# Performance work log

Measured on AMD Instinct MI355X. Metric: run time of the kernel, lower is better.

The kernel has to match this reference:

```python
import jax, jax.numpy as jnp
import numpy as np

K = 3        # neighborhood kernel per spatial dim
DIL = 1      # dilation per spatial dim
NH = 8       # num heads
C = 64       # embed dims
EPS = 1e-5   # InstanceNorm eps


def _interp_axis(x, axis, out_len):
    # 1D linear interpolation with align_corners=True semantics
    in_len = x.shape[axis]
    pos = jnp.arange(out_len, dtype=jnp.float32) * ((in_len - 1) / (out_len - 1))
    i0 = jnp.clip(jnp.floor(pos).astype(jnp.int32), 0, in_len - 2)
    w = pos - i0.astype(jnp.float32)
    shape = [1] * x.ndim
    shape[axis] = out_len
    w = w.reshape(shape)
    return jnp.take(x, i0, axis=axis) * (1.0 - w) + jnp.take(x, i0 + 1, axis=axis) * w


def _upsample2_trilinear(x):
    # separable trilinear upsample x2 over the three spatial axes (2,3,4)
    for ax in (2, 3, 4):
        x = _interp_axis(x, ax, 2 * x.shape[ax])
    return x


def _instance_norm(t):
    # InstanceNorm3d, affine=False: normalize per (B,C) over spatial dims
    m = jnp.mean(t, axis=(2, 3, 4), keepdims=True)
    v = jnp.var(t, axis=(2, 3, 4), keepdims=True)
    return (t - m) * jax.lax.rsqrt(v + EPS)


def _nbr_idx(L, k, d):
    # NATTEN-style clamped neighborhood: window shifts to stay in-bounds at edges
    i = np.arange(L)
    start = np.clip(i - d * (k // 2), 0, L - d * (k - 1) - 1)
    idx = start[:, None] + np.arange(k)[None, :] * d          # (L,k) absolute nbr index
    rel = (idx - i[:, None]) // d + (k - 1)                   # (L,k) rel-pos-bias index in [0,2k-2]
    return jnp.asarray(idx), jnp.asarray(rel)


def _nca3d(qs, kv, Wq, bq, Wk, bk, Wv, bv, Wo, bo, rpb):
    # qs, kv: (B,H,W,Z,C) channels-last; q from skip, k/v from upsampled x
    B, H, W, Z, Cc = qs.shape
    dh = Cc // NH
    scale = dh ** -0.5
    q = (qs @ Wq + bq).reshape(B, H, W, Z, NH, dh) * scale
    k = (kv @ Wk + bk).reshape(B, H, W, Z, NH, dh)
    v = (kv @ Wv + bv).reshape(B, H, W, Z, NH, dh)

    ih, rh = _nbr_idx(H, K, DIL)
    iw, rw = _nbr_idx(W, K, DIL)
    iz, rz = _nbr_idx(Z, K, DIL)

    def gather_nbrs(t):
        t = jnp.take(t, ih, axis=1)   # (B,H,k,W,Z,nh,dh)
        t = jnp.take(t, iw, axis=3)   # (B,H,k,W,k,Z,nh,dh)
        t = jnp.take(t, iz, axis=5)   # (B,H,k,W,k,Z,k,nh,dh)
        t = jnp.transpose(t, (0, 1, 3, 5, 7, 2, 4, 6, 8))
        return t.reshape(B, H, W, Z, NH, K * K * K, dh)

    kg = gather_nbrs(k)
    vg = gather_nbrs(v)

    logits = jnp.einsum('bxyzhd,bxyzhmd->bxyzhm', q, kg)  # (B,H,W,Z,nh,27)

    # relative position bias: rpb (nh, 2k-1, 2k-1, 2k-1) gathered per query position
    bias = rpb[:, rh]                    # (nh,H,k,2k-1,2k-1)
    bias = jnp.take(bias, rw, axis=3)    # (nh,H,k,W,k,2k-1)
    bias = jnp.take(bias, rz, axis=5)    # (nh,H,k,W,k,Z,k)
    bias = jnp.transpose(bias, (1, 3, 5, 0, 2, 4, 6)).reshape(H, W, Z, NH, K * K * K)

    attn = jax.nn.softmax(logits + bias, axis=-1)
    o = jnp.einsum('bxyzhm,bxyzhmd->bxyzhd', attn, vg).reshape(B, H, W, Z, Cc)
    o = o @ Wo + bo
    return jnp.transpose(o, (0, 4, 1, 2, 3))  # back to (B,C,H,W,Z)


def setup_inputs() -> dict:
    key = jax.random.key(0)
    ks = jax.random.split(key, 8)
    s = 1.0 / np.sqrt(C)
    inp = {
        'x': jax.random.normal(ks[0], (1, C, 32, 32, 8), dtype=jnp.float32),
        'skip': jax.random.normal(ks[1], (1, C, 64, 64, 16), dtype=jnp.float32),
        'Wq': jax.random.normal(ks[2], (C, C), dtype=jnp.float32) * s,
        'bq': jnp.zeros((C,), dtype=jnp.float32),
        'Wk': jax.random.normal(ks[3], (C, C), dtype=jnp.float32) * s,
        'bk': jnp.zeros((C,), dtype=jnp.float32),
        'Wv': jax.random.normal(ks[4], (C, C), dtype=jnp.float32) * s,
        'bv': jnp.zeros((C,), dtype=jnp.float32),
        'Wo': jax.random.normal(ks[5], (C, C), dtype=jnp.float32) * s,
        'bo': jnp.zeros((C,), dtype=jnp.float32),
        'rpb': jax.random.normal(ks[6], (NH, 2 * K - 1, 2 * K - 1, 2 * K - 1), dtype=jnp.float32) * 0.02,
    }
    return inp


def reference(x, skip, Wq, bq, Wk, bk, Wv, bv, Wo, bo, rpb):
    xu = _instance_norm(_upsample2_trilinear(x))   # (B,C,2H,2W,2Z) == skip shape
    sk = _instance_norm(skip)
    qs = jnp.transpose(sk, (0, 2, 3, 4, 1))        # queries from skip
    kv = jnp.transpose(xu, (0, 2, 3, 4, 1))        # keys/values from upsampled x
    return _nca3d(qs, kv, Wq, bq, Wk, bk, Wv, bv, Wo, bo, rpb)
```

## Files before the change

kernel.cpp:

```cpp
#include <hip/hip_runtime.h>
#include <hip/hip_bf16.h>

typedef __hip_bfloat16 bf16;
typedef __attribute__((ext_vector_type(8))) short short8;

static constexpr int NPOS = 65536;

__device__ __forceinline__ float bs2f(short s) {
  union { float f; unsigned u; } cv;
  cv.u = ((unsigned)(unsigned short)s) << 16;
  return cv.f;
}
__device__ __forceinline__ short f2bs(float f) {
  bf16 b = __float2bfloat16(f);
  short r;
  __builtin_memcpy(&r, &b, 2);
  return r;
}

__global__ __launch_bounds__(256) void k_partial(const float* __restrict__ x,
                                                 const float* __restrict__ skip,
                                                 bf16* __restrict__ xu,
                                                 float* __restrict__ partials) {
  __shared__ float s1[256];
  __shared__ float s2[256];
  int b = blockIdx.x, tid = threadIdx.x;
  float sum = 0.f, sq = 0.f;
  if (b < 1024) {
    int c = b >> 4;
    int h = (b & 15) * 4 + (tid >> 6);
    int w = tid & 63;
    float fh = (float)h * (31.0f / 63.0f);
    int ih = (int)fh; if (ih > 30) ih = 30;
    float wh = fh - (float)ih;
    float fw = (float)w * (31.0f / 63.0f);
    int iw = (int)fw; if (iw > 30) iw = 30;
    float ww = fw - (float)iw;
    const float* base = x + c * 8192 + ih * 256 + iw * 8;
    float4 A0 = *(const float4*)(base);
    float4 A1 = *(const float4*)(base + 4);
    float4 B0 = *(const float4*)(base + 8);
    float4 B1 = *(const float4*)(base + 12);
    float4 C0 = *(const float4*)(base + 256);
    float4 C1 = *(const float4*)(base + 260);
    float4 D0 = *(const float4*)(base + 264);
    float4 D1 = *(const float4*)(base + 268);
    float ra[8] = {A0.x, A0.y, A0.z, A0.w, A1.x, A1.y, A1.z, A1.w};
    float rb[8] = {B0.x, B0.y, B0.z, B0.w, B1.x, B1.y, B1.z, B1.w};
    float rc[8] = {C0.x, C0.y, C0.z, C0.w, C1.x, C1.y, C1.z, C1.w};
    float rd[8] = {D0.x, D0.y, D0.z, D0.w, D1.x, D1.y, D1.z, D1.w};
    short8 o0, o1;
#pragma unroll
    for (int z = 0; z < 16; z++) {
      float fz = (float)z * (7.0f / 15.0f);
      int iz = (int)fz; if (iz > 6) iz = 6;
      float wz = fz - (float)iz;
      float va = ra[iz] * (1.f - wz) + ra[iz + 1] * wz;
      float vb = rb[iz] * (1.f - wz) + rb[iz + 1] * wz;
      float vc = rc[iz] * (1.f - wz) + rc[iz + 1] * wz;
      float vd = rd[iz] * (1.f - wz) + rd[iz + 1] * wz;
      float v0 = va * (1.f - ww) + vb * ww;
      float v1 = vc * (1.f - ww) + vd * ww;
      float v = v0 * (1.f - wh) + v1 * wh;
      sum += v; sq += v * v;
      if (z < 8) o0[z] = f2bs(v); else o1[z - 8] = f2bs(v);
    }
    bf16* xo = xu + (size_t)c * NPOS + h * 1024 + w * 16;
    *(short8*)xo = o0;
    *(short8*)(xo + 8) = o1;
  } else {
    int bb = b - 1024;
    const float4* p =
        (const float4*)(skip + (size_t)(bb >> 4) * NPOS + (bb & 15) * 4096);
    for (int i = tid; i < 1024; i += 256) {
      float4 v = p[i];
      sum += v.x + v.y + v.z + v.w;
      sq += v.x * v.x + v.y * v.y + v.z * v.z + v.w * v.w;
    }
  }
  s1[tid] = sum; s2[tid] = sq;
  __syncthreads();
  for (int s = 128; s > 0; s >>= 1) {
    if (tid < s) { s1[tid] += s1[tid + s]; s2[tid] += s2[tid + s]; }
    __syncthreads();
  }
  if (tid == 0) { partials[2 * b] = s1[0]; partials[2 * b + 1] = s2[0]; }
}

__global__ __launch_bounds__(128) void k_finalize(const float* __restrict__ partials,
                                                  float* __restrict__ stats) {
  int t = threadIdx.x;
  int base = (t < 64) ? t * 16 : 1024 + (t - 64) * 16;
  float sum = 0.f, sq = 0.f;
#pragma unroll
  for (int j = 0; j < 16; j++) {
    sum += partials[2 * (base + j)];
    sq  += partials[2 * (base + j) + 1];
  }
  float m = sum * (1.0f / NPOS);
  float var = sq * (1.0f / NPOS) - m * m;
  int off = (t < 64) ? 0 : 128;
  int c = t & 63;
  stats[off + c] = m;
  stats[off + 64 + c] = rsqrtf(var + 1e-5f);
}

__global__ __launch_bounds__(256) void k_proj_kvq(
    const bf16* __restrict__ xu, const float* __restrict__ skip,
    const float* __restrict__ stats,
    const float* __restrict__ Wk, const float* __restrict__ bk,
    const float* __restrict__ Wv, const float* __restrict__ bv,
    const float* __restrict__ Wq, const float* __restrict__ bq,
    bf16* __restrict__ kbuf, bf16* __restrict__ vbuf, bf16* __restrict__ qbuf) {
  __shared__ float xt[4096];
  int tid = threadIdx.x;
  int p0 = blockIdx.x * 64;
  for (int ii = tid; ii < 512; ii += 256) {
    int c = ii >> 3, t0 = (ii & 7) * 8;
    short8 v8 = *(const short8*)(xu + (size_t)c * NPOS + p0 + t0);
    float m = stats[c], r = stats[64 + c];
#pragma unroll
    for (int u = 0; u < 8; u++) xt[c * 64 + t0 + u] = (bs2f(v8[u]) - m) * r;
  }
  __syncthreads();
  int t = tid & 63;
  int j0 = __builtin_amdgcn_readfirstlane((tid >> 6) * 16);
  size_t p = (size_t)(p0 + t);
  float a[16];
  short8 s0, s1v;

#pragma unroll
  for (int u = 0; u < 16; u++) a[u] = bk[j0 + u];
  for (int c = 0; c < 64; c++) {
    float xv = xt[c * 64 + t];
    const float* wr = Wk + c * 64 + j0;
#pragma unroll
    for (int u = 0; u < 16; u++) a[u] += xv * wr[u];
  }
#pragma unroll
  for (int u = 0; u < 8; u++) { s0[u] = f2bs(a[u]); s1v[u] = f2bs(a[8 + u]); }
  *(short8*)(kbuf + p * 64 + j0) = s0;
  *(short8*)(kbuf + p * 64 + j0 + 8) = s1v;

#pragma unroll
  for (int u = 0; u < 16; u++) a[u] = bv[j0 + u];
  for (int c = 0; c < 64; c++) {
    float xv = xt[c * 64 + t];
    const float* wr = Wv + c * 64 + j0;
#pragma unroll
    for (int u = 0; u < 16; u++) a[u] += xv * wr[u];
  }
#pragma unroll
  for (int u = 0; u < 8; u++) { s0[u] = f2bs(a[u]); s1v[u] = f2bs(a[8 + u]); }
  *(short8*)(vbuf + p * 64 + j0) = s0;
  *(short8*)(vbuf + p * 64 + j0 + 8) = s1v;

  __syncthreads();
  for (int ii = tid; ii < 1024; ii += 256) {
    int c = ii >> 4, t0 = (ii & 15) * 4;
    float4 v = *(const float4*)(skip + (size_t)c * NPOS + p0 + t0);
    float m = stats[128 + c], r = stats[192 + c];
    xt[c * 64 + t0]     = (v.x - m) * r;
    xt[c * 64 + t0 + 1] = (v.y - m) * r;
    xt[c * 64 + t0 + 2] = (v.z - m) * r;
    xt[c * 64 + t0 + 3] = (v.w - m) * r;
  }
  __syncthreads();

  const float scale = 0.35355339059327373f;
#pragma unroll
  for (int u = 0; u < 16; u++) a[u] = bq[j0 + u];
  for (int c = 0; c < 64; c++) {
    float xv = xt[c * 64 + t];
    const float* wr = Wq + c * 64 + j0;
#pragma unroll
    for (int u = 0; u < 16; u++) a[u] += xv * wr[u];
  }
#pragma unroll
  for (int u = 0; u < 8; u++) {
    s0[u] = f2bs(a[u] * scale); s1v[u] = f2bs(a[8 + u] * scale);
  }
  *(short8*)(qbuf + p * 64 + j0) = s0;
  *(short8*)(qbuf + p * 64 + j0 + 8) = s1v;
}

__global__ __launch_bounds__(512, 2) void k_attn(
    const bf16* __restrict__ qbuf, const bf16* __restrict__ kbuf,
    const bf16* __restrict__ vbuf,
    const float* __restrict__ Wo, const float* __restrict__ bo,
    const float* __restrict__ rpb, float* __restrict__ out) {
  __shared__ float rp[1000];
  __shared__ float oT[64 * 65];
  int tid = threadIdx.x;
  int b = blockIdx.x;
  int sb = ((b & 7) << 7) + (b >> 3);
  int p0 = sb * 64;
  for (int i = tid; i < 1000; i += 512) rp[i] = rpb[i];
  __syncthreads();

  int head = tid & 7, pp = tid >> 3;
  int p = p0 + pp;
  int h = p >> 10, w = (p >> 4) & 63, z = p & 15;

  short8 q8 = *(const short8*)(qbuf + (size_t)p * 64 + head * 8);
  float q[8];
#pragma unroll
  for (int d = 0; d < 8; d++) q[d] = bs2f(q8[d]);

  int sh = h - 1; if (sh < 0) sh = 0; if (sh > 61) sh = 61;
  int sw = w - 1; if (sw < 0) sw = 0; if (sw > 61) sw = 61;
  int sz = z - 1; if (sz < 0) sz = 0; if (sz > 13) sz = 13;

  const bf16* kb = kbuf + (size_t)(sh * 1024 + sw * 16 + sz) * 64 + head * 8;
  const bf16* vb = vbuf + (size_t)(sh * 1024 + sw * 16 + sz) * 64 + head * 8;
  int rbase = ((sh - h + 2) * 5 + (sw - w + 2)) * 5 + (sz - z + 2) + head * 125;

  float s[27];
#pragma unroll
  for (int j = 0; j < 27; j++) {
    int kh = j / 9, kw = (j % 9) / 3, kz = j % 3;
    int coff = (kh * 1024 + kw * 16 + kz) * 64;
    short8 k8 = *(const short8*)(kb + coff);
    float sv = q[0] * bs2f(k8[0]) + q[1] * bs2f(k8[1]) +
               q[2] * bs2f(k8[2]) + q[3] * bs2f(k8[3]) +
               q[4] * bs2f(k8[4]) + q[5] * bs2f(k8[5]) +
               q[6] * bs2f(k8[6]) + q[7] * bs2f(k8[7]);
    s[j] = sv + rp[rbase + (kh * 5 + kw) * 5 + kz];
  }
  float M = s[26];
#pragma unroll
  for (int j = 0; j < 13; j++) M = fmaxf(M, fmaxf(s[2 * j], s[2 * j + 1]));

  float lrun = 0.f;
  float oa[8];
#pragma unroll
  for (int d = 0; d < 8; d++) oa[d] = 0.f;
#pragma unroll
  for (int j = 0; j < 27; j++) {
    int kh = j / 9, kw = (j % 9) / 3, kz = j % 3;
    int coff = (kh * 1024 + kw * 16 + kz) * 64;
    short8 v8 = *(const short8*)(vb + coff);
    float pw = __expf(s[j] - M);
    lrun += pw;
#pragma unroll
    for (int d = 0; d < 8; d++) oa[d] += pw * bs2f(v8[d]);
  }
  float inv = 1.0f / lrun;
#pragma unroll
  for (int d = 0; d < 8; d++) oT[pp * 65 + head * 8 + d] = oa[d] * inv;
  __syncthreads();

  int wid = __builtin_amdgcn_readfirstlane(tid >> 6);
  int l = tid & 63;
  float acc[8];
#pragma unroll
  for (int u = 0; u < 8; u++) acc[u] = bo[wid * 8 + u];
  for (int j = 0; j < 64; j++) {
    float ov = oT[l * 65 + j];
    const float* wr = Wo + j * 64 + wid * 8;
#pragma unroll
    for (int u = 0; u < 8; u++) acc[u] += ov * wr[u];
  }
#pragma unroll
  for (int u = 0; u < 8; u++)
    out[(size_t)(wid * 8 + u) * NPOS + p0 + l] = acc[u];
}

extern "C" void kernel_launch(void* const* d_in, const int* in_sizes, int n_in,
                              void* d_out, int out_size, void* d_ws, size_t ws_size,
                              hipStream_t stream) {
  const float* x    = (const float*)d_in[0];
  const float* skip = (const float*)d_in[1];
  const float* Wq   = (const float*)d_in[2];
  const float* bq   = (const float*)d_in[3];
  const float* Wk   = (const float*)d_in[4];
  const float* bk   = (const float*)d_in[5];
  const float* Wv   = (const float*)d_in[6];
  const float* bv   = (const float*)d_in[7];
  const float* Wo   = (const float*)d_in[8];
  const float* bo   = (const float*)d_in[9];
  const float* rpb  = (const float*)d_in[10];

  bf16* xu        = (bf16*)d_ws;
  bf16* kbuf      = (bf16*)((char*)d_ws + ((size_t)8 << 20));
  bf16* vbuf      = (bf16*)((char*)d_ws + ((size_t)16 << 20));
  bf16* qbuf      = (bf16*)((char*)d_ws + ((size_t)24 << 20));
  float* stats    = (float*)((char*)d_ws + ((size_t)32 << 20));
  float* partials = stats + 256;
  float* out = (float*)d_out;

  hipLaunchKernelGGL(k_partial, dim3(2048), dim3(256), 0, stream, x, skip, xu,
                     partials);
  hipLaunchKernelGGL(k_finalize, dim3(1), dim3(128), 0, stream, partials, stats);
  hipLaunchKernelGGL(k_proj_kvq, dim3(1024), dim3(256), 0, stream, xu, skip,
                     stats, Wk, bk, Wv, bv, Wq, bq, kbuf, vbuf, qbuf);
  hipLaunchKernelGGL(k_attn, dim3(1024), dim3(512), 0, stream, qbuf, kbuf, vbuf,
                     Wo, bo, rpb, out);
}
```

Measured before the change: 159.7 us.

## Fuse all stages into one persistent kernel with grid barriers and MFMA projections

Replaces the four launches with a single persistent 256-block kernel that uses atomic grid-wide barriers between the statistics, projection and attention phases. The Q/K/V projections move from scalar FMA to bf16 MFMA with weights staged in LDS, and Wo is cached in LDS for the output projection. The aim is to cut launch overhead and per-block reloads of weights. The risks are low occupancy, since only 256 blocks at one block per SM do all the attention work, and that the spin barrier can deadlock if not all blocks are co-resident.

```diff
diff --git a/kernel.cpp b/kernel.cpp
--- a/kernel.cpp
+++ b/kernel.cpp
@@ -3,6 +3,7 @@
 
 typedef __hip_bfloat16 bf16;
 typedef __attribute__((ext_vector_type(8))) short short8;
+typedef __attribute__((ext_vector_type(4))) float f32x4;
 
 static constexpr int NPOS = 65536;
 
@@ -18,252 +19,305 @@
   return r;
 }
 
-__global__ __launch_bounds__(256) void k_partial(const float* __restrict__ x,
-                                                 const float* __restrict__ skip,
-                                                 bf16* __restrict__ xu,
-                                                 float* __restrict__ partials) {
-  __shared__ float s1[256];
-  __shared__ float s2[256];
-  int b = blockIdx.x, tid = threadIdx.x;
+__device__ __forceinline__ void gbar(unsigned* ctr, unsigned nblk) {
+  __syncthreads();
+  if (threadIdx.x == 0) {
+    __threadfence();
+    __hip_atomic_fetch_add(ctr, 1u, __ATOMIC_RELEASE, __HIP_MEMORY_SCOPE_AGENT);
+    while (__hip_atomic_load(ctr, __ATOMIC_ACQUIRE, __HIP_MEMORY_SCOPE_AGENT) <
+           nblk) {
+      __builtin_amdgcn_s_sleep(8);
+    }
+    __threadfence();
+  }
+  __syncthreads();
+}
+
+__global__ void k_init(unsigned* bar) {
+  if (threadIdx.x < 8) bar[threadIdx.x] = 0u;
+}
+
+__device__ __forceinline__ void upsample_col(const float* __restrict__ xc,
+                                             int h, int w, float& sum,
+                                             float& sq, bf16* __restrict__ xo) {
+  float fh = (float)h * (31.0f / 63.0f);
+  int ih = (int)fh; if (ih > 30) ih = 30;
+  float wh = fh - (float)ih;
+  float fw = (float)w * (31.0f / 63.0f);
+  int iw = (int)fw; if (iw > 30) iw = 30;
+  float ww = fw - (float)iw;
+  const float* base = xc + ih * 256 + iw * 8;
+  float4 A0 = *(const float4*)(base);
+  float4 A1 = *(const float4*)(base + 4);
+  float4 B0 = *(const float4*)(base + 8);
+  float4 B1 = *(const float4*)(base + 12);
+  float4 C0 = *(const float4*)(base + 256);
+  float4 C1 = *(const float4*)(base + 260);
+  float4 D0 = *(const float4*)(base + 264);
+  float4 D1 = *(const float4*)(base + 268);
+  float ra[8] = {A0.x, A0.y, A0.z, A0.w, A1.x, A1.y, A1.z, A1.w};
+  float rb[8] = {B0.x, B0.y, B0.z, B0.w, B1.x, B1.y, B1.z, B1.w};
+  float rc[8] = {C0.x, C0.y, C0.z, C0.w, C1.x, C1.y, C1.z, C1.w};
+  float rd[8] = {D0.x, D0.y, D0.z, D0.w, D1.x, D1.y, D1.z, D1.w};
+  short8 o0, o1;
+#define ZSTEP(zz)                                                              \
+  {                                                                            \
+    constexpr float fz = (float)(zz) * (7.0f / 15.0f);                         \
+    constexpr int izr = (int)fz;                                               \
+    constexpr int iz = (izr > 6) ? 6 : izr;                                    \
+    constexpr float wz = fz - (float)iz;                                       \
+    float va = ra[iz] * (1.f - wz) + ra[iz + 1] * wz;                          \
+    float vb = rb[iz] * (1.f - wz) + rb[iz + 1] * wz;                          \
+    float vc = rc[iz] * (1.f - wz) + rc[iz + 1] * wz;                          \
+    float vd = rd[iz] * (1.f - wz) + rd[iz + 1] * wz;                          \
+    float v0 = va * (1.f - ww) + vb * ww;                                      \
+    float v1 = vc * (1.f - ww) + vd * ww;                                      \
+    float v = v0 * (1.f - wh) + v1 * wh;                                       \
+    sum += v; sq += v * v;                                                     \
+    if ((zz) < 8) o0[(zz) & 7] = f2bs(v); else o1[(zz) & 7] = f2bs(v);         \
+  }
+  ZSTEP(0) ZSTEP(1) ZSTEP(2) ZSTEP(3) ZSTEP(4) ZSTEP(5) ZSTEP(6) ZSTEP(7)
+  ZSTEP(8) ZSTEP(9) ZSTEP(10) ZSTEP(11) ZSTEP(12) ZSTEP(13) ZSTEP(14) ZSTEP(15)
+#undef ZSTEP
+  *(short8*)xo = o0;
+  *(short8*)(xo + 8) = o1;
+}
+
+__global__ __launch_bounds__(256, 1) void k_fused(
+    const float* __restrict__ x, const float* __restrict__ skip,
+    const float* __restrict__ Wq, const float* __restrict__ bq,
+    const float* __restrict__ Wk, const float* __restrict__ bk,
+    const float* __restrict__ Wv, const float* __restrict__ bv,
+    const float* __restrict__ Wo, const float* __restrict__ bo,
+    const float* __restrict__ rpb,
+    bf16* __restrict__ xu, bf16* __restrict__ kbuf, bf16* __restrict__ vbuf,
+    bf16* __restrict__ qbuf, float* __restrict__ partials,
+    unsigned* __restrict__ bar, float* __restrict__ out) {
+  __shared__ float stl[256];
+  __shared__ float red1[256];
+  __shared__ float red2[256];
+  __shared__ float bol[64];
+  __shared__ __align__(16) char scratch[47104];
+  int tid = threadIdx.x, b = blockIdx.x;
+
   float sum = 0.f, sq = 0.f;
-  if (b < 1024) {
-    int c = b >> 4;
-    int h = (b & 15) * 4 + (tid >> 6);
-    int w = tid & 63;
-    float fh = (float)h * (31.0f / 63.0f);
-    int ih = (int)fh; if (ih > 30) ih = 30;
-    float wh = fh - (float)ih;
-    float fw = (float)w * (31.0f / 63.0f);
-    int iw = (int)fw; if (iw > 30) iw = 30;
-    float ww = fw - (float)iw;
-    const float* base = x + c * 8192 + ih * 256 + iw * 8;
-    float4 A0 = *(const float4*)(base);
-    float4 A1 = *(const float4*)(base + 4);
-    float4 B0 = *(const float4*)(base + 8);
-    float4 B1 = *(const float4*)(base + 12);
-    float4 C0 = *(const float4*)(base + 256);
-    float4 C1 = *(const float4*)(base + 260);
-    float4 D0 = *(const float4*)(base + 264);
-    float4 D1 = *(const float4*)(base + 268);
-    float ra[8] = {A0.x, A0.y, A0.z, A0.w, A1.x, A1.y, A1.z, A1.w};
-    float rb[8] = {B0.x, B0.y, B0.z, B0.w, B1.x, B1.y, B1.z, B1.w};
-    float rc[8] = {C0.x, C0.y, C0.z, C0.w, C1.x, C1.y, C1.z, C1.w};
-    float rd[8] = {D0.x, D0.y, D0.z, D0.w, D1.x, D1.y, D1.z, D1.w};
-    short8 o0, o1;
-#pragma unroll
-    for (int z = 0; z < 16; z++) {
-      float fz = (float)z * (7.0f / 15.0f);
-      int iz = (int)fz; if (iz > 6) iz = 6;
-      float wz = fz - (float)iz;
-      float va = ra[iz] * (1.f - wz) + ra[iz + 1] * wz;
-      float vb = rb[iz] * (1.f - wz) + rb[iz + 1] * wz;
-      float vc = rc[iz] * (1.f - wz) + rc[iz + 1] * wz;
-      float vd = rd[iz] * (1.f - wz) + rd[iz + 1] * wz;
-      float v0 = va * (1.f - ww) + vb * ww;
-      float v1 = vc * (1.f - ww) + vd * ww;
-      float v = v0 * (1.f - wh) + v1 * wh;
-      sum += v; sq += v * v;
-      if (z < 8) o0[z] = f2bs(v); else o1[z - 8] = f2bs(v);
-    }
-    bf16* xo = xu + (size_t)c * NPOS + h * 1024 + w * 16;
-    *(short8*)xo = o0;
-    *(short8*)(xo + 8) = o1;
+  if (b < 128) {
+    int c = b >> 1, hh = (b & 1) * 32;
+    const float* xc = x + c * 8192;
+    bf16* xo = xu + (size_t)c * NPOS;
+#pragma unroll
+    for (int i = 0; i < 8; i++) {
+      int col = i * 256 + tid;
+      int h = hh + (col >> 6), w = col & 63;
+      upsample_col(xc, h, w, sum, sq, xo + h * 1024 + w * 16);
+    }
   } else {
-    int bb = b - 1024;
+    int bb = b - 128, c = bb >> 1;
     const float4* p =
-        (const float4*)(skip + (size_t)(bb >> 4) * NPOS + (bb & 15) * 4096);
-    for (int i = tid; i < 1024; i += 256) {
-      float4 v = p[i];
+        (const float4*)(skip + (size_t)c * NPOS + (bb & 1) * 32768);
+#pragma unroll 4
+    for (int k = 0; k < 32; k++) {
+      float4 v = p[k * 256 + tid];
       sum += v.x + v.y + v.z + v.w;
       sq += v.x * v.x + v.y * v.y + v.z * v.z + v.w * v.w;
     }
   }
-  s1[tid] = sum; s2[tid] = sq;
+  red1[tid] = sum; red2[tid] = sq;
   __syncthreads();
   for (int s = 128; s > 0; s >>= 1) {
-    if (tid < s) { s1[tid] += s1[tid + s]; s2[tid] += s2[tid + s]; }
-    __syncthreads();
-  }
-  if (tid == 0) { partials[2 * b] = s1[0]; partials[2 * b + 1] = s2[0]; }
-}
-
-__global__ __launch_bounds__(128) void k_finalize(const float* __restrict__ partials,
-                                                  float* __restrict__ stats) {
-  int t = threadIdx.x;
-  int base = (t < 64) ? t * 16 : 1024 + (t - 64) * 16;
-  float sum = 0.f, sq = 0.f;
-#pragma unroll
-  for (int j = 0; j < 16; j++) {
-    sum += partials[2 * (base + j)];
-    sq  += partials[2 * (base + j) + 1];
-  }
-  float m = sum * (1.0f / NPOS);
-  float var = sq * (1.0f / NPOS) - m * m;
-  int off = (t < 64) ? 0 : 128;
-  int c = t & 63;
-  stats[off + c] = m;
-  stats[off + 64 + c] = rsqrtf(var + 1e-5f);
-}
-
-__global__ __launch_bounds__(256) void k_proj_kvq(
-    const bf16* __restrict__ xu, const float* __restrict__ skip,
-    const float* __restrict__ stats,
-    const float* __restrict__ Wk, const float* __restrict__ bk,
-    const float* __restrict__ Wv, const float* __restrict__ bv,
-    const float* __restrict__ Wq, const float* __restrict__ bq,
-    bf16* __restrict__ kbuf, bf16* __restrict__ vbuf, bf16* __restrict__ qbuf) {
-  __shared__ float xt[4096];
-  int tid = threadIdx.x;
-  int p0 = blockIdx.x * 64;
-  for (int ii = tid; ii < 512; ii += 256) {
-    int c = ii >> 3, t0 = (ii & 7) * 8;
-    short8 v8 = *(const short8*)(xu + (size_t)c * NPOS + p0 + t0);
-    float m = stats[c], r = stats[64 + c];
-#pragma unroll
-    for (int u = 0; u < 8; u++) xt[c * 64 + t0 + u] = (bs2f(v8[u]) - m) * r;
-  }
-  __syncthreads();
-  int t = tid & 63;
-  int j0 = __builtin_amdgcn_readfirstlane((tid >> 6) * 16);
-  size_t p = (size_t)(p0 + t);
-  float a[16];
-  short8 s0, s1v;
-
-#pragma unroll
-  for (int u = 0; u < 16; u++) a[u] = bk[j0 + u];
-  for (int c = 0; c < 64; c++) {
-    float xv = xt[c * 64 + t];
-    const float* wr = Wk + c * 64 + j0;
-#pragma unroll
-    for (int u = 0; u < 16; u++) a[u] += xv * wr[u];
-  }
-#pragma unroll
-  for (int u = 0; u < 8; u++) { s0[u] = f2bs(a[u]); s1v[u] = f2bs(a[8 + u]); }
-  *(short8*)(kbuf + p * 64 + j0) = s0;
-  *(short8*)(kbuf + p * 64 + j0 + 8) = s1v;
-
-#pragma unroll
-  for (int u = 0; u < 16; u++) a[u] = bv[j0 + u];
-  for (int c = 0; c < 64; c++) {
-    float xv = xt[c * 64 + t];
-    const float* wr = Wv + c * 64 + j0;
-#pragma unroll
-    for (int u = 0; u < 16; u++) a[u] += xv * wr[u];
-  }
-#pragma unroll
-  for (int u = 0; u < 8; u++) { s0[u] = f2bs(a[u]); s1v[u] = f2bs(a[8 + u]); }
-  *(short8*)(vbuf + p * 64 + j0) = s0;
-  *(short8*)(vbuf + p * 64 + j0 + 8) = s1v;
-
-  __syncthreads();
-  for (int ii = tid; ii < 1024; ii += 256) {
-    int c = ii >> 4, t0 = (ii & 15) * 4;
-    float4 v = *(const float4*)(skip + (size_t)c * NPOS + p0 + t0);
-    float m = stats[128 + c], r = stats[192 + c];
-    xt[c * 64 + t0]     = (v.x - m) * r;
-    xt[c * 64 + t0 + 1] = (v.y - m) * r;
-    xt[c * 64 + t0 + 2] = (v.z - m) * r;
-    xt[c * 64 + t0 + 3] = (v.w - m) * r;
-  }
-  __syncthreads();
-
+    if (tid < s) { red1[tid] += red1[tid + s]; red2[tid] += red2[tid + s]; }
+    __syncthreads();
+  }
+  if (tid == 0) { partials[2 * b] = red1[0]; partials[2 * b + 1] = red2[0]; }
+
+  gbar(bar + 0, 256);
+
+  if (tid < 128) {
+    int isk = tid >> 6, c = tid & 63;
+    int b0 = isk ? (128 + 2 * c) : (2 * c);
+    float s_ = partials[2 * b0] + partials[2 * b0 + 2];
+    float q_ = partials[2 * b0 + 1] + partials[2 * b0 + 3];
+    float m = s_ * (1.0f / NPOS);
+    float var = q_ * (1.0f / NPOS) - m * m;
+    stl[isk * 128 + c] = m;
+    stl[isk * 128 + 64 + c] = rsqrtf(var + 1e-5f);
+  }
+  if (tid < 64) bol[tid] = bo[tid];
+
+  short* xa  = (short*)scratch;
+  short* ob  = (short*)(scratch + 9216);
+  short* wbk = (short*)(scratch + 18432);
+  short* wbv = (short*)(scratch + 27648);
+  short* wbq = (short*)(scratch + 36864);
+  {
+    int c = tid >> 2, j0 = (tid & 3) * 16;
+#define LOADW(dst, W)                                                          \
+    {                                                                          \
+      const float4* wr = (const float4*)((W) + c * 64 + j0);                   \
+      float4 w0 = wr[0], w1 = wr[1], w2 = wr[2], w3 = wr[3];                   \
+      float wv16[16] = {w0.x, w0.y, w0.z, w0.w, w1.x, w1.y, w1.z, w1.w,        \
+                        w2.x, w2.y, w2.z, w2.w, w3.x, w3.y, w3.z, w3.w};       \
+      _Pragma("unroll") for (int u = 0; u < 16; u++)                           \
+          dst[(j0 + u) * 72 + c] = f2bs(wv16[u]);                              \
+    }
+    LOADW(wbk, Wk)
+    LOADW(wbv, Wv)
+    LOADW(wbq, Wq)
+#undef LOADW
+  }
+  __syncthreads();
+
+  int wv_ = tid >> 6, lane = tid & 63, quad = lane >> 4, l15 = lane & 15;
+  int orow0 = wv_ * 16 + quad * 4;
   const float scale = 0.35355339059327373f;
-#pragma unroll
-  for (int u = 0; u < 16; u++) a[u] = bq[j0 + u];
-  for (int c = 0; c < 64; c++) {
-    float xv = xt[c * 64 + t];
-    const float* wr = Wq + c * 64 + j0;
-#pragma unroll
-    for (int u = 0; u < 16; u++) a[u] += xv * wr[u];
-  }
-#pragma unroll
-  for (int u = 0; u < 8; u++) {
-    s0[u] = f2bs(a[u] * scale); s1v[u] = f2bs(a[8 + u] * scale);
-  }
-  *(short8*)(qbuf + p * 64 + j0) = s0;
-  *(short8*)(qbuf + p * 64 + j0 + 8) = s1v;
-}
-
-__global__ __launch_bounds__(512, 2) void k_attn(
-    const bf16* __restrict__ qbuf, const bf16* __restrict__ kbuf,
-    const bf16* __restrict__ vbuf,
-    const float* __restrict__ Wo, const float* __restrict__ bo,
-    const float* __restrict__ rpb, float* __restrict__ out) {
-  __shared__ float rp[1000];
-  __shared__ float oT[64 * 65];
-  int tid = threadIdx.x;
-  int b = blockIdx.x;
-  int sb = ((b & 7) << 7) + (b >> 3);
-  int p0 = sb * 64;
-  for (int i = tid; i < 1000; i += 512) rp[i] = rpb[i];
+
+  for (int t = 0; t < 4; t++) {
+    int tile = ((b & 7) << 7) + ((b >> 3) << 2) + t;
+    int p0 = tile * 64;
+    for (int ii = tid; ii < 512; ii += 256) {
+      int c = ii >> 3, t0 = (ii & 7) * 8;
+      short8 v8 = *(const short8*)(xu + (size_t)c * NPOS + p0 + t0);
+      float m = stl[c], r = stl[64 + c];
+#pragma unroll
+      for (int u = 0; u < 8; u++)
+        xa[(t0 + u) * 72 + c] = f2bs((bs2f(v8[u]) - m) * r);
+    }
+    __syncthreads();
+    const short* arow = &xa[(wv_ * 16 + l15) * 72 + quad * 8];
+#define MFMA_PASS(WB, BIAS, SC)                                                \
+    {                                                                          \
+      short8 a0 = *(const short8*)(arow);                                      \
+      short8 a1 = *(const short8*)(arow + 32);                                 \
+      _Pragma("unroll") for (int nt = 0; nt < 4; nt++) {                       \
+        const short* brow = &WB[(nt * 16 + l15) * 72 + quad * 8];              \
+        short8 b0 = *(const short8*)(brow);                                    \
+        short8 b1 = *(const short8*)(brow + 32);                               \
+        f32x4 acc = {0.f, 0.f, 0.f, 0.f};                                      \
+        acc = __builtin_amdgcn_mfma_f32_16x16x32_bf16(a0, b0, acc, 0, 0, 0);   \
+        acc = __builtin_amdgcn_mfma_f32_16x16x32_bf16(a1, b1, acc, 0, 0, 0);   \
+        float bval = BIAS[nt * 16 + l15];                                      \
+        _Pragma("unroll") for (int r = 0; r < 4; r++)                          \
+            ob[(orow0 + r) * 72 + nt * 16 + l15] = f2bs((acc[r] + bval) * SC); \
+      }                                                                        \
+    }
+#define STORE_OB(DST)                                                          \
+    {                                                                          \
+      int row = tid >> 2, col0 = (tid & 3) * 16;                               \
+      short8 o0 = *(const short8*)(&ob[row * 72 + col0]);                      \
+      short8 o1 = *(const short8*)(&ob[row * 72 + col0 + 8]);                  \
+      *(short8*)(DST + (size_t)(p0 + row) * 64 + col0) = o0;                   \
+      *(short8*)(DST + (size_t)(p0 + row) * 64 + col0 + 8) = o1;               \
+    }
+    MFMA_PASS(wbk, bk, 1.0f)
+    __syncthreads();
+    STORE_OB(kbuf)
+    __syncthreads();
+    MFMA_PASS(wbv, bv, 1.0f)
+    __syncthreads();
+    STORE_OB(vbuf)
+    for (int ii = tid; ii < 1024; ii += 256) {
+      int c = ii >> 4, t0 = (ii & 15) * 4;
+      float4 v = *(const float4*)(skip + (size_t)c * NPOS + p0 + t0);
+      float m = stl[128 + c], r = stl[192 + c];
+      xa[(t0 + 0) * 72 + c] = f2bs((v.x - m) * r);
+      xa[(t0 + 1) * 72 + c] = f2bs((v.y - m) * r);
+      xa[(t0 + 2) * 72 + c] = f2bs((v.z - m) * r);
+      xa[(t0 + 3) * 72 + c] = f2bs((v.w - m) * r);
+    }
+    __syncthreads();
+    MFMA_PASS(wbq, bq, scale)
+    __syncthreads();
+    STORE_OB(qbuf)
+    __syncthreads();
+#undef MFMA_PASS
+#undef STORE_OB
+  }
+
+  gbar(bar + 1, 256);
+
+  float* rp = (float*)scratch;
+  float* wo = (float*)(scratch + 4000);
+  float* oT = (float*)(scratch + 20384);
+  for (int i = tid; i < 1000; i += 256) rp[i] = rpb[i];
+  for (int i = tid; i < 1024; i += 256)
+    ((float4*)wo)[i] = ((const float4*)Wo)[i];
   __syncthreads();
 
   int head = tid & 7, pp = tid >> 3;
-  int p = p0 + pp;
-  int h = p >> 10, w = (p >> 4) & 63, z = p & 15;
-
-  short8 q8 = *(const short8*)(qbuf + (size_t)p * 64 + head * 8);
-  float q[8];
-#pragma unroll
-  for (int d = 0; d < 8; d++) q[d] = bs2f(q8[d]);
-
-  int sh = h - 1; if (sh < 0) sh = 0; if (sh > 61) sh = 61;
-  int sw = w - 1; if (sw < 0) sw = 0; if (sw > 61) sw = 61;
-  int sz = z - 1; if (sz < 0) sz = 0; if (sz > 13) sz = 13;
-
-  const bf16* kb = kbuf + (size_t)(sh * 1024 + sw * 16 + sz) * 64 + head * 8;
-  const bf16* vb = vbuf + (size_t)(sh * 1024 + sw * 16 + sz) * 64 + head * 8;
-  int rbase = ((sh - h + 2) * 5 + (sw - w + 2)) * 5 + (sz - z + 2) + head * 125;
-
-  float s[27];
-#pragma unroll
-  for (int j = 0; j < 27; j++) {
-    int kh = j / 9, kw = (j % 9) / 3, kz = j % 3;
-    int coff = (kh * 1024 + kw * 16 + kz) * 64;
-    short8 k8 = *(const short8*)(kb + coff);
-    float sv = q[0] * bs2f(k8[0]) + q[1] * bs2f(k8[1]) +
-               q[2] * bs2f(k8[2]) + q[3] * bs2f(k8[3]) +
-               q[4] * bs2f(k8[4]) + q[5] * bs2f(k8[5]) +
-               q[6] * bs2f(k8[6]) + q[7] * bs2f(k8[7]);
-    s[j] = sv + rp[rbase + (kh * 5 + kw) * 5 + kz];
-  }
-  float M = s[26];
-#pragma unroll
-  for (int j = 0; j < 13; j++) M = fmaxf(M, fmaxf(s[2 * j], s[2 * j + 1]));
-
-  float lrun = 0.f;
-  float oa[8];
-#pragma unroll
-  for (int d = 0; d < 8; d++) oa[d] = 0.f;
-#pragma unroll
-  for (int j = 0; j < 27; j++) {
-    int kh = j / 9, kw = (j % 9) / 3, kz = j % 3;
-    int coff = (kh * 1024 + kw * 16 + kz) * 64;
-    short8 v8 = *(const short8*)(vb + coff);
-    float pw = __expf(s[j] - M);
-    lrun += pw;
-#pragma unroll
-    for (int d = 0; d < 8; d++) oa[d] += pw * bs2f(v8[d]);
-  }
-  float inv = 1.0f / lrun;
-#pragma unroll
-  for (int d = 0; d < 8; d++) oT[pp * 65 + head * 8 + d] = oa[d] * inv;
-  __syncthreads();
-
-  int wid = __builtin_amdgcn_readfirstlane(tid >> 6);
-  int l = tid & 63;
-  float acc[8];
-#pragma unroll
-  for (int u = 0; u < 8; u++) acc[u] = bo[wid * 8 + u];
-  for (int j = 0; j < 64; j++) {
-    float ov = oT[l * 65 + j];
-    const float* wr = Wo + j * 64 + wid * 8;
-#pragma unroll
-    for (int u = 0; u < 8; u++) acc[u] += ov * wr[u];
-  }
-#pragma unroll
-  for (int u = 0; u < 8; u++)
-    out[(size_t)(wid * 8 + u) * NPOS + p0 + l] = acc[u];
+  for (int t = 0; t < 4; t++) {
+    int tile = ((b & 7) << 7) + ((b >> 3) << 2) + t;
+    for (int half = 0; half < 2; half++) {
+      int p = tile * 64 + half * 32 + pp;
+      int h = p >> 10, w = (p >> 4) & 63, z = p & 15;
+      short8 q8 = *(const short8*)(qbuf + (size_t)p * 64 + head * 8);
+      float q[8];
+#pragma unroll
+      for (int d = 0; d < 8; d++) q[d] = bs2f(q8[d]);
+      int sh = h - 1; if (sh < 0) sh = 0; if (sh > 61) sh = 61;
+      int sw = w - 1; if (sw < 0) sw = 0; if (sw > 61) sw = 61;
+      int sz = z - 1; if (sz < 0) sz = 0; if (sz > 13) sz = 13;
+      const bf16* kb = kbuf + (size_t)(sh * 1024 + sw * 16 + sz) * 64 + head * 8;
+      const bf16* vb = vbuf + (size_t)(sh * 1024 + sw * 16 + sz) * 64 + head * 8;
+      int rbase =
+          ((sh - h + 2) * 5 + (sw - w + 2)) * 5 + (sz - z + 2) + head * 125;
+      float s[27];
+#pragma unroll
+      for (int j = 0; j < 27; j++) {
+        int kh = j / 9, kw = (j % 9) / 3, kz = j % 3;
+        int coff = (kh * 1024 + kw * 16 + kz) * 64;
+        short8 k8 = *(const short8*)(kb + coff);
+        float sv = q[0] * bs2f(k8[0]) + q[1] * bs2f(k8[1]) +
+                   q[2] * bs2f(k8[2]) + q[3] * bs2f(k8[3]) +
+                   q[4] * bs2f(k8[4]) + q[5] * bs2f(k8[5]) +
+                   q[6] * bs2f(k8[6]) + q[7] * bs2f(k8[7]);
+        s[j] = sv + rp[rbase + (kh * 5 + kw) * 5 + kz];
+      }
+      float M = s[26];
+#pragma unroll
+      for (int j = 0; j < 13; j++) M = fmaxf(M, fmaxf(s[2 * j], s[2 * j + 1]));
+      float lrun = 0.f;
+      float oa[8];
+#pragma unroll
+      for (int d = 0; d < 8; d++) oa[d] = 0.f;
+#pragma unroll
+      for (int j = 0; j < 27; j++) {
+        int kh = j / 9, kw = (j % 9) / 3, kz = j % 3;
+        int coff = (kh * 1024 + kw * 16 + kz) * 64;
+        short8 v8 = *(const short8*)(vb + coff);
+        float pw = __expf(s[j] - M);
+        lrun += pw;
+#pragma unroll
+        for (int d = 0; d < 8; d++) oa[d] += pw * bs2f(v8[d]);
+      }
+      float inv = 1.0f / lrun;
+#pragma unroll
+      for (int d = 0; d < 8; d++)
+        oT[(half * 32 + pp) * 65 + head * 8 + d] = oa[d] * inv;
+    }
+    __syncthreads();
+    int wid = tid >> 6, l = tid & 63;
+    int p0 = tile * 64;
+    float acc[16];
+#pragma unroll
+    for (int u = 0; u < 16; u++) acc[u] = bol[wid * 16 + u];
+    for (int j = 0; j < 64; j++) {
+      float ov = oT[l * 65 + j];
+      const float4* wr4 = (const float4*)&wo[j * 64 + wid * 16];
+      float4 w0 = wr4[0], w1 = wr4[1], w2 = wr4[2], w3 = wr4[3];
+      acc[0] += ov * w0.x;  acc[1] += ov * w0.y;
+      acc[2] += ov * w0.z;  acc[3] += ov * w0.w;
+      acc[4] += ov * w1.x;  acc[5] += ov * w1.y;
+      acc[6] += ov * w1.z;  acc[7] += ov * w1.w;
+      acc[8] += ov * w2.x;  acc[9] += ov * w2.y;
+      acc[10] += ov * w2.z; acc[11] += ov * w2.w;
+      acc[12] += ov * w3.x; acc[13] += ov * w3.y;
+      acc[14] += ov * w3.z; acc[15] += ov * w3.w;
+    }
+#pragma unroll
+    for (int u = 0; u < 16; u++)
+      out[(size_t)(wid * 16 + u) * NPOS + p0 + l] = acc[u];
+    __syncthreads();
+  }
 }
 
 extern "C" void kernel_launch(void* const* d_in, const int* in_sizes, int n_in,
@@ -285,15 +339,12 @@
   bf16* kbuf      = (bf16*)((char*)d_ws + ((size_t)8 << 20));
   bf16* vbuf      = (bf16*)((char*)d_ws + ((size_t)16 << 20));
   bf16* qbuf      = (bf16*)((char*)d_ws + ((size_t)24 << 20));
-  float* stats    = (float*)((char*)d_ws + ((size_t)32 << 20));
-  float* partials = stats + 256;
+  float* partials = (float*)((char*)d_ws + ((size_t)32 << 20));
+  unsigned* bar   = (unsigned*)((char*)d_ws + ((size_t)32 << 20) + 4096);
   float* out = (float*)d_out;
 
-  hipLaunchKernelGGL(k_partial, dim3(2048), dim3(256), 0, stream, x, skip, xu,
-                     partials);
-  hipLaunchKernelGGL(k_finalize, dim3(1), dim3(128), 0, stream, partials, stats);
-  hipLaunchKernelGGL(k_proj_kvq, dim3(1024), dim3(256), 0, stream, xu, skip,
-                     stats, Wk, bk, Wv, bv, Wq, bq, kbuf, vbuf, qbuf);
-  hipLaunchKernelGGL(k_attn, dim3(1024), dim3(512), 0, stream, qbuf, kbuf, vbuf,
-                     Wo, bo, rpb, out);
-}
+  hipLaunchKernelGGL(k_init, dim3(1), dim3(64), 0, stream, bar);
+  hipLaunchKernelGGL(k_fused, dim3(256), dim3(256), 0, stream, x, skip, Wq, bq,
+                     Wk, bk, Wv, bv, Wo, bo, rpb, xu, kbuf, vbuf, qbuf,
+                     partials, bar, out);
+}
```

After: 226.1 us. 41.6% more time.
